# Kernel optimization log

Measured on AMD Instinct MI355X. Metric: run time of the kernel, lower is better.

Reference implementation:

```python
import jax, jax.numpy as jnp
import numpy as np

N, E, F_IN, HID, HEADS, NCLS, NG = 50000, 800000, 128, 128, 4, 10, 512
C = HID // HEADS          # per-head channels
BN_EPS = 1e-5
NEG_SLOPE = 0.2           # SuperGATConv default negative_slope
N_CONV = 3


def setup_inputs() -> dict:
    key = jax.random.key(0)
    ks = jax.random.split(key, 16)
    x = jax.random.normal(ks[0], (N, F_IN), jnp.float32)
    # edges with no self loops (reference appends self loops itself, as SuperGATConv does)
    src = jax.random.randint(ks[1], (E,), 0, N, dtype=jnp.int32)
    off = jax.random.randint(ks[2], (E,), 1, N, dtype=jnp.int32)
    dst = (src + off) % N
    edge_index = jnp.stack([src, dst], axis=0)
    batch = jnp.sort(jax.random.randint(ks[3], (N,), 0, NG, dtype=jnp.int32))
    s = 0.1
    # BatchNorm params per module init: weight=1, bias=1e-4 (running stats fresh: mean=0, var=1)
    inp = {
        "x": x, "edge_index": edge_index, "batch": batch,
        "bn_feat_g": jnp.ones((F_IN,), jnp.float32), "bn_feat_b": jnp.full((F_IN,), 1e-4, jnp.float32),
        "w_feat": jax.random.normal(ks[4], (F_IN, HID), jnp.float32) * s,
        "b_feat": jnp.zeros((HID,), jnp.float32),
        "bn_conv_g": jnp.ones((N_CONV, HID), jnp.float32), "bn_conv_b": jnp.full((N_CONV, HID), 1e-4, jnp.float32),
        "w_gat": jax.random.normal(ks[5], (N_CONV, HID, HID), jnp.float32) * s,
        "att_l": jax.random.normal(ks[6], (N_CONV, HEADS, C), jnp.float32) * s,
        "att_r": jax.random.normal(ks[7], (N_CONV, HEADS, C), jnp.float32) * s,
        "b_gat": jnp.zeros((N_CONV, HID), jnp.float32),
        "bn_fc_g": jnp.ones((HID,), jnp.float32), "bn_fc_b": jnp.full((HID,), 1e-4, jnp.float32),
        "w_fc": jax.random.normal(ks[8], (HID, HID), jnp.float32) * s,
        "b_fc": jnp.zeros((HID,), jnp.float32),
        "bn_hid_g": jnp.ones((HID,), jnp.float32), "bn_hid_b": jnp.full((HID,), 1e-4, jnp.float32),
        "w_cls": jax.random.normal(ks[9], (HID, NCLS), jnp.float32) * s,
        "b_cls": jnp.zeros((NCLS,), jnp.float32),
    }
    return inp


def _bn_eval(h, g, b):
    # eval-mode BatchNorm1d with fresh running stats (mean=0, var=1)
    return h * (g / jnp.sqrt(1.0 + BN_EPS)) + b


def _segment_softmax(a, seg, num_segments):
    # softmax over edges grouped by destination node (PyG softmax semantics)
    m = jax.ops.segment_max(a, seg, num_segments=num_segments)
    a = jnp.exp(a - m[seg])
    s = jax.ops.segment_sum(a, seg, num_segments=num_segments)
    return a / (s[seg] + 1e-16)


def _supergat_mx(h, src, dst, W, att_l, att_r, bias):
    # h: [N, HID] -> per-head features [N, H, C]
    hh = (h @ W).reshape(N, HEADS, C)
    h_j = hh[src]  # source (message) features  [E2, H, C]
    h_i = hh[dst]  # destination features       [E2, H, C]
    logits = jnp.einsum('ehc,ehc->eh', h_i, h_j)                       # MX dot-product
    alpha = jnp.einsum('ehc,hc->eh', h_j, att_l) + jnp.einsum('ehc,hc->eh', h_i, att_r)
    alpha = alpha * jax.nn.sigmoid(logits)
    alpha = jax.nn.leaky_relu(alpha, NEG_SLOPE)
    alpha = _segment_softmax(alpha, dst, N)                            # [E2, H]
    out = jax.ops.segment_sum(h_j * alpha[..., None], dst, num_segments=N)
    return out.reshape(N, HID) + bias


def reference(x, edge_index, batch, bn_feat_g, bn_feat_b, w_feat, b_feat,
              bn_conv_g, bn_conv_b, w_gat, att_l, att_r, b_gat,
              bn_fc_g, bn_fc_b, w_fc, b_fc, bn_hid_g, bn_hid_b, w_cls, b_cls):
    loops = jnp.arange(N, dtype=edge_index.dtype)
    src = jnp.concatenate([edge_index[0], loops])   # SuperGATConv adds self loops
    dst = jnp.concatenate([edge_index[1], loops])
    h = _bn_eval(x, bn_feat_g, bn_feat_b)
    h = jax.nn.relu(h @ w_feat + b_feat)            # GCNConv(gfn=True) == Linear
    for i in range(N_CONV):
        h = _bn_eval(h, bn_conv_g[i], bn_conv_b[i])
        h = jax.nn.relu(_supergat_mx(h, src, dst, w_gat[i], att_l[i], att_r[i], b_gat[i]))
    g = jax.ops.segment_sum(h, batch, num_segments=NG)  # global_add_pool -> [NG, HID]
    g = _bn_eval(g, bn_fc_g, bn_fc_b)
    g = jax.nn.relu(g @ w_fc + b_fc)
    g = _bn_eval(g, bn_hid_g, bn_hid_b)
    logits = g @ w_cls + b_cls
    att_loss = jnp.float32(0.0)  # eval mode: no edge-sampled attention loss
    return jax.nn.log_softmax(logits, axis=-1), att_loss
```

## Files before the change

### kernel.cpp

```cpp
#include <hip/hip_runtime.h>

#define NN 50000
#define EE 800000
#define FHID 128
#define NHEAD 4
#define NGRAPH 512
#define NCLS 10
#define BK 256
#define BCH 4096
#define NBLK_E 196
#define NBUCK 196
#define CAPB 6144

typedef unsigned short u16;
typedef unsigned int u32;
typedef unsigned long long u64;
typedef __attribute__((ext_vector_type(8))) short bf16x8;
typedef __attribute__((ext_vector_type(4))) float f32x4;

__device__ __forceinline__ float bf2f(u16 u){
    union { u32 i; float f; } v; v.i = ((u32)u) << 16; return v.f;
}
__device__ __forceinline__ float bflo(u32 u){
    union { u32 i; float f; } v; v.i = u << 16; return v.f;
}
__device__ __forceinline__ float bfhi(u32 u){
    union { u32 i; float f; } v; v.i = u & 0xffff0000u; return v.f;
}
__device__ __forceinline__ u16 f2bf(float f){
    union { float f; u32 i; } v; v.f = f;
    u32 r = v.i + 0x7fffu + ((v.i >> 16) & 1u);
    return (u16)(r >> 16);
}
__device__ __forceinline__ u32 pack2(float a, float b){
    return ((u32)f2bf(b) << 16) | f2bf(a);
}
__device__ __forceinline__ float loadF(const void* p, int i, int isf32){
    return isf32 ? ((const float*)p)[i] : bf2f(((const u16*)p)[i]);
}
__device__ __forceinline__ void unpk8(uint4 v, float* f){
    f[0]=bflo(v.x); f[1]=bfhi(v.x);
    f[2]=bflo(v.y); f[3]=bfhi(v.y);
    f[4]=bflo(v.z); f[5]=bfhi(v.z);
    f[6]=bflo(v.w); f[7]=bfhi(v.w);
}

__device__ int detect_local(const u16* x, int tid, int nthreads, int* lds){
    int ok = 0;
    for (int i = tid; i < 1024; i += nthreads){
        u16 u = x[i];
        int e = (u >> 7) & 0xFF;
        if ((u & 0x7fff) == 0 || (e >= 0x70 && e <= 0x85)) ok++;
    }
    lds[tid] = ok;
    __syncthreads();
    for (int o2 = nthreads >> 1; o2 > 0; o2 >>= 1){
        if (tid < o2) lds[tid] += lds[tid + o2];
        __syncthreads();
    }
    int r = (lds[0] < 900) ? 1 : 0;
    __syncthreads();
    return r;
}

__global__ __launch_bounds__(256) void prep_all(
        const u16* __restrict__ xz,
        const void* w_feat, const void* b_feat, const void* bn_feat_g, const void* bn_feat_b,
        const void* w_gat, const void* bn_conv_g, const void* bn_conv_b, const void* b_gat,
        const void* wfc, const void* bfc, const void* bnfg, const void* bnfb,
        const void* bnhg, const void* bnhb, const void* wcls, const void* bcls,
        const void* attl, const void* attr,
        u16* __restrict__ Wt, float* __restrict__ cvec, float* __restrict__ biasv,
        float* __restrict__ hp, int* __restrict__ dflag, int* __restrict__ gcur)
{
    __shared__ int ldsi[256];
    __shared__ float red[128];
    int bid = blockIdx.x, t = threadIdx.x;
    int isf32 = detect_local(xz, t, 256, ldsi);
    if (bid == 0){
        if (t == 0) dflag[0] = isf32;
        gcur[t] = t * CAPB;
    }

    if (bid < 512){
        if (t >= 128) return;
        int L = bid >> 7;
        int n = bid & 127;
        int k = t;
        const float rs = rsqrtf(1.0f + 1e-5f);
        float wv, bg, bb;
        if (L == 0){
            wv = loadF(w_feat, k*FHID + n, isf32);
            bg = loadF(bn_feat_g, k, isf32);
            bb = loadF(bn_feat_b, k, isf32);
        } else {
            wv = loadF(w_gat, (L-1)*FHID*FHID + k*FHID + n, isf32);
            bg = loadF(bn_conv_g, (L-1)*FHID + k, isf32);
            bb = loadF(bn_conv_b, (L-1)*FHID + k, isf32);
        }
        Wt[L*FHID*FHID + n*FHID + k] = f2bf(bg * rs * wv);
        red[k] = bb * wv;
        __syncthreads();
        for (int o2 = 64; o2 > 0; o2 >>= 1){
            if (k < o2) red[k] += red[k + o2];
            __syncthreads();
        }
        if (k == 0){
            float c = red[0];
            if (L == 0) c += loadF(b_feat, n, isf32);
            cvec[L*FHID + n] = c;
            if (L > 0) biasv[L*FHID + n] = loadF(b_gat, (L-1)*FHID + n, isf32);
        }
    } else {
        int gt = (bid - 512)*256 + t;
        for (int i = gt; i < FHID*FHID; i += 16*256) hp[i] = loadF(wfc, i, isf32);
        if (gt < FHID*NCLS) hp[16384 + gt] = loadF(wcls, gt, isf32);
        if (gt >= 2048 && gt < 2048 + 3*FHID){
            int i = gt - 2048;
            hp[18320 + i] = loadF(attl, i, isf32);
            hp[18704 + i] = loadF(attr, i, isf32);
        }
        if (gt >= 2560 && gt < 2560 + FHID){
            int tt = gt - 2560;
            hp[17664 + tt] = loadF(bnfg, tt, isf32);
            hp[17792 + tt] = loadF(bnfb, tt, isf32);
            hp[17920 + tt] = loadF(bfc,  tt, isf32);
            hp[18048 + tt] = loadF(bnhg, tt, isf32);
            hp[18176 + tt] = loadF(bnhb, tt, isf32);
        }
        if (gt >= 3072 && gt < 3072 + NCLS) hp[18304 + (gt - 3072)] = loadF(bcls, gt - 3072, isf32);
    }
}

__global__ __launch_bounds__(256) void gemm128(const void* __restrict__ A,
                                               const u16* __restrict__ Wt,
                                               const float* __restrict__ cvec,
                                               u16* __restrict__ out, int relu,
                                               int araw, const int* __restrict__ flag,
                                               const float* __restrict__ attl,
                                               const float* __restrict__ attr,
                                               float* __restrict__ al,
                                               float* __restrict__ ar)
{
    int wave = threadIdx.x >> 6;
    int lane = threadIdx.x & 63;
    int m = lane & 15, quad = lane >> 4;
    int rowbase = blockIdx.x * 128 + wave * 32;
    bool f32in = araw && flag[0];
    const u16*  Au = (const u16*)A;
    const float* Af = (const float*)A;
    int r0 = rowbase + m, r1 = rowbase + 16 + m;
    bool v0 = r0 < NN, v1 = r1 < NN;
    f32x4 acc[2][8];
#pragma unroll
    for (int i = 0; i < 2; i++)
#pragma unroll
        for (int j = 0; j < 8; j++) acc[i][j] = (f32x4){0.f,0.f,0.f,0.f};
#pragma unroll
    for (int t = 0; t < 4; t++){
        bf16x8 a0 = {0,0,0,0,0,0,0,0}, a1 = {0,0,0,0,0,0,0,0};
        int kof = t*32 + quad*8;
        if (f32in){
            if (v0){
                const float* p = Af + (size_t)r0*FHID + kof;
                float4 u0 = *(const float4*)p, u1 = *(const float4*)(p+4);
                a0[0]=(short)f2bf(u0.x); a0[1]=(short)f2bf(u0.y);
                a0[2]=(short)f2bf(u0.z); a0[3]=(short)f2bf(u0.w);
                a0[4]=(short)f2bf(u1.x); a0[5]=(short)f2bf(u1.y);
                a0[6]=(short)f2bf(u1.z); a0[7]=(short)f2bf(u1.w);
            }
            if (v1){
                const float* p = Af + (size_t)r1*FHID + kof;
                float4 u0 = *(const float4*)p, u1 = *(const float4*)(p+4);
                a1[0]=(short)f2bf(u0.x); a1[1]=(short)f2bf(u0.y);
                a1[2]=(short)f2bf(u0.z); a1[3]=(short)f2bf(u0.w);
                a1[4]=(short)f2bf(u1.x); a1[5]=(short)f2bf(u1.y);
                a1[6]=(short)f2bf(u1.z); a1[7]=(short)f2bf(u1.w);
            }
        } else {
            if (v0) a0 = *(const bf16x8*)(Au + (size_t)r0*FHID + kof);
            if (v1) a1 = *(const bf16x8*)(Au + (size_t)r1*FHID + kof);
        }
#pragma unroll
        for (int ct = 0; ct < 8; ct++){
            bf16x8 wfrag = *(const bf16x8*)(Wt + (ct*16 + m)*FHID + kof);
            acc[0][ct] = __builtin_amdgcn_mfma_f32_16x16x32_bf16(wfrag, a0, acc[0][ct], 0, 0, 0);
            acc[1][ct] = __builtin_amdgcn_mfma_f32_16x16x32_bf16(wfrag, a1, acc[1][ct], 0, 0, 0);
        }
    }
    bool doa = (attl != nullptr);
#pragma unroll
    for (int tt = 0; tt < 2; tt++){
        int row = rowbase + tt*16 + m;
        bool rv = row < NN;
        float sl[4] = {0.f,0.f,0.f,0.f};
        float sr[4] = {0.f,0.f,0.f,0.f};
#pragma unroll
        for (int ct = 0; ct < 8; ct++){
            int cb = ct*16 + quad*4;
            float4 cv = *(const float4*)(cvec + cb);
            float w0 = acc[tt][ct][0] + cv.x;
            float w1 = acc[tt][ct][1] + cv.y;
            float w2 = acc[tt][ct][2] + cv.z;
            float w3 = acc[tt][ct][3] + cv.w;
            if (relu){
                w0 = fmaxf(w0, 0.f); w1 = fmaxf(w1, 0.f);
                w2 = fmaxf(w2, 0.f); w3 = fmaxf(w3, 0.f);
            }
            if (doa){
                int h = ct >> 1;
                float4 tl = *(const float4*)(attl + cb);
                float4 tr = *(const float4*)(attr + cb);
                sl[h] += w0*tl.x + w1*tl.y + w2*tl.z + w3*tl.w;
                sr[h] += w0*tr.x + w1*tr.y + w2*tr.z + w3*tr.w;
            }
            if (rv){
                uint2 st; st.x = pack2(w0, w1); st.y = pack2(w2, w3);
                *(uint2*)(out + (size_t)row*FHID + cb) = st;
            }
        }
        if (doa){
#pragma unroll
            for (int h = 0; h < 4; h++){
                sl[h] += __shfl_xor(sl[h], 16, 64);
                sl[h] += __shfl_xor(sl[h], 32, 64);
                sr[h] += __shfl_xor(sr[h], 16, 64);
                sr[h] += __shfl_xor(sr[h], 32, 64);
            }
            if (rv){
                al[row*NHEAD + quad] = sl[quad];
                ar[row*NHEAD + quad] = sr[quad];
            }
        }
    }
}

__global__ __launch_bounds__(256) void bin_edges(const int* __restrict__ srcp,
        const int* __restrict__ dstp, int* __restrict__ gcur, u64* __restrict__ binned)
{
    __shared__ int h[BK], lb[BK], gb[BK], cur[BK];
    __shared__ u64 stage[BCH];
    int t = threadIdx.x;
    h[t] = 0;
    __syncthreads();
    int base = blockIdx.x * BCH;
    int sv[16], dv[16];
#pragma unroll
    for (int k = 0; k < 16; k++){
        int e = base + k*256 + t;
        int d = -1, s = 0;
        if (e < EE){
            d = dstp[e]; s = srcp[e];
            if ((u32)d >= NN) d = -1;
        }
        sv[k] = s; dv[k] = d;
        if (d >= 0) atomicAdd(&h[d >> 8], 1);
    }
    __syncthreads();
    lb[t] = h[t];
    __syncthreads();
    for (int off = 1; off < BK; off <<= 1){
        int x = (t >= off) ? lb[t - off] : 0;
        __syncthreads();
        lb[t] += x;
        __syncthreads();
    }
    int excl = lb[t] - h[t];
    int tot  = lb[BK-1];
    __syncthreads();
    lb[t] = excl;
    gb[t] = h[t] ? atomicAdd(&gcur[t], h[t]) : 0;
    cur[t] = 0;
    __syncthreads();
#pragma unroll
    for (int k = 0; k < 16; k++){
        int d = dv[k];
        if (d >= 0){
            int b = d >> 8;
            int p = lb[b] + atomicAdd(&cur[b], 1);
            stage[p] = ((u64)(u32)d << 32) | (u32)sv[k];
        }
    }
    __syncthreads();
    for (int i = t; i < tot; i += 256){
        u64 pr = stage[i];
        int b = (int)(pr >> 40);
        binned[gb[b] + (i - lb[b])] = pr;
    }
}

__global__ __launch_bounds__(256) void build_csr(const u64* __restrict__ binned,
        const int* __restrict__ gcur, int2* __restrict__ rowdeg, int* __restrict__ colbuf)
{
    __shared__ int deg[BK], ls[BK], cur[BK];
    __shared__ int colstage[CAPB];
    int b = blockIdx.x, t = threadIdx.x;
    int gb = b * CAPB;
    int cnt = gcur[b] - gb;
    if (cnt < 0) cnt = 0;
    if (cnt > CAPB) cnt = CAPB;
    deg[t] = 0;
    __syncthreads();
    for (int i = t; i < cnt; i += 256){
        int d = (int)(binned[gb + i] >> 32);
        atomicAdd(&deg[d & 255], 1);
    }
    __syncthreads();
    ls[t] = deg[t];
    __syncthreads();
    for (int off = 1; off < BK; off <<= 1){
        int x = (t >= off) ? ls[t - off] : 0;
        __syncthreads();
        ls[t] += x;
        __syncthreads();
    }
    int excl = ls[t] - deg[t];
    int node = b*256 + t;
    if (node < NN) rowdeg[node] = (int2){gb + excl, gb + excl + deg[t]};
    cur[t] = excl;
    __syncthreads();
    for (int i = t; i < cnt; i += 256){
        u64 pr = binned[gb + i];
        int d = (int)(pr >> 32) & 255;
        int s = (int)(u32)pr;
        int p = atomicAdd(&cur[d], 1);
        colstage[p] = s;
    }
    __syncthreads();
    for (int i = t; i < cnt; i += 256) colbuf[gb + i] = colstage[i];
}

__global__ __launch_bounds__(256) void supergat_conv(const u16* __restrict__ hh,
        const float* __restrict__ al, const float* __restrict__ ar,
        const int2* __restrict__ rowdeg, const int* __restrict__ colbuf,
        const float* __restrict__ bias, u16* __restrict__ hout)
{
    int wid  = (blockIdx.x*256 + threadIdx.x) >> 6;
    int lane = threadIdx.x & 63;
    int group = lane >> 4;
    int gl    = lane & 15;
    int head  = gl >> 2;
    int q     = gl & 3;
    int node  = wid*4 + group;
    bool valid = node < NN;
    int snode = valid ? node : 0;
    int chbase = head*32 + q*8;

    uint4 hdv = *(const uint4*)(hh + (size_t)snode*FHID + chbase);
    float hd[8]; unpk8(hdv, hd);
    float arn = ar[snode*NHEAD + head];
    float aln = al[snode*NHEAD + head];

    float d = hd[0]*hd[0]+hd[1]*hd[1]+hd[2]*hd[2]+hd[3]*hd[3]
            + hd[4]*hd[4]+hd[5]*hd[5]+hd[6]*hd[6]+hd[7]*hd[7];
    d += __shfl_xor(d, 1, 64);
    d += __shfl_xor(d, 2, 64);
    float a = (aln + arn) * (1.0f / (1.0f + __expf(-d)));
    a = (a > 0.0f) ? a : 0.2f*a;
    float p = __expf(fminf(a, 60.f));
    float s = p;
    float o[8];
#pragma unroll
    for (int i = 0; i < 8; i++) o[i] = p*hd[i];

    int2 rd = valid ? rowdeg[node] : (int2){0,0};
    int e0 = rd.x, e1 = rd.y;
    if (e0 < 0) e0 = 0;
    if (e1 > BK*CAPB) e1 = BK*CAPB;

    int e = e0;
    while (e + 3 < e1){
        int sidx[4]; uint4 xv[4]; float af[4];
#pragma unroll
        for (int j = 0; j < 4; j++){
            int si = colbuf[e + j];
            if ((u32)si >= NN) si = 0;
            sidx[j] = si;
        }
#pragma unroll
        for (int j = 0; j < 4; j++){
            xv[j] = *(const uint4*)(hh + (size_t)sidx[j]*FHID + chbase);
            af[j] = al[sidx[j]*NHEAD + head];
        }
#pragma unroll
        for (int j = 0; j < 4; j++){
            float hs[8]; unpk8(xv[j], hs);
            float lg = hd[0]*hs[0]+hd[1]*hs[1]+hd[2]*hs[2]+hd[3]*hs[3]
                     + hd[4]*hs[4]+hd[5]*hs[5]+hd[6]*hs[6]+hd[7]*hs[7];
            lg += __shfl_xor(lg, 1, 64);
            lg += __shfl_xor(lg, 2, 64);
            float a2 = (af[j] + arn) * (1.0f / (1.0f + __expf(-lg)));
            a2 = (a2 > 0.0f) ? a2 : 0.2f*a2;
            float pe = __expf(fminf(a2, 60.f));
            s += pe;
#pragma unroll
            for (int i = 0; i < 8; i++) o[i] += pe*hs[i];
        }
        e += 4;
    }
    while (e < e1){
        int si = colbuf[e];
        if ((u32)si >= NN) si = 0;
        uint4 x1 = *(const uint4*)(hh + (size_t)si*FHID + chbase);
        float af1 = al[si*NHEAD + head];
        float hs[8]; unpk8(x1, hs);
        float lg = hd[0]*hs[0]+hd[1]*hs[1]+hd[2]*hs[2]+hd[3]*hs[3]
                 + hd[4]*hs[4]+hd[5]*hs[5]+hd[6]*hs[6]+hd[7]*hs[7];
        lg += __shfl_xor(lg, 1, 64);
        lg += __shfl_xor(lg, 2, 64);
        float a2 = (af1 + arn) * (1.0f / (1.0f + __expf(-lg)));
        a2 = (a2 > 0.0f) ? a2 : 0.2f*a2;
        float pe = __expf(fminf(a2, 60.f));
        s += pe;
#pragma unroll
        for (int i = 0; i < 8; i++) o[i] += pe*hs[i];
        e++;
    }

    if (valid){
        float inv = 1.0f / (s + 1e-16f);
        uint4 w;
        w.x = pack2(fmaxf(o[0]*inv + bias[chbase+0], 0.f),
                    fmaxf(o[1]*inv + bias[chbase+1], 0.f));
        w.y = pack2(fmaxf(o[2]*inv + bias[chbase+2], 0.f),
                    fmaxf(o[3]*inv + bias[chbase+3], 0.f));
        w.z = pack2(fmaxf(o[4]*inv + bias[chbase+4], 0.f),
                    fmaxf(o[5]*inv + bias[chbase+5], 0.f));
        w.w = pack2(fmaxf(o[6]*inv + bias[chbase+6], 0.f),
                    fmaxf(o[7]*inv + bias[chbase+7], 0.f));
        *(uint4*)(hout + (size_t)node*FHID + chbase) = w;
    }
}

__global__ void pool_head(const u16* __restrict__ h, const int* __restrict__ batch,
                          const float* __restrict__ hp, const int* __restrict__ flag,
                          void* __restrict__ out)
{
    __shared__ int bounds[2];
    __shared__ float gb[FHID];
    __shared__ float g2[FHID];
    __shared__ float lg[16];
    int gi = blockIdx.x, t = threadIdx.x;
    int isf32 = flag[0];
    if (t < 2){
        int target = gi + t;
        int lo = 0, hi = NN;
        while (lo < hi){
            int mid = (lo + hi) >> 1;
            if (batch[mid] < target) lo = mid + 1; else hi = mid;
        }
        bounds[t] = lo;
    }
    __syncthreads();
    float acc0 = 0.f;
    for (int node = bounds[0]; node < bounds[1]; node++)
        acc0 += bf2f(h[(size_t)node*FHID + t]);
    const float rs = rsqrtf(1.0f + 1e-5f);
    gb[t] = acc0 * (hp[17664 + t] * rs) + hp[17792 + t];
    __syncthreads();
    float acc = hp[17920 + t];
    for (int k = 0; k < FHID; k++) acc += gb[k] * hp[k*FHID + t];
    acc = fmaxf(acc, 0.f);
    g2[t] = acc * (hp[18048 + t] * rs) + hp[18176 + t];
    __syncthreads();
    if (t < NCLS){
        float l = hp[18304 + t];
        for (int k = 0; k < FHID; k++) l += g2[k] * hp[16384 + k*NCLS + t];
        lg[t] = l;
    }
    __syncthreads();
    if (t == 0){
        float mx = lg[0];
        for (int j = 1; j < NCLS; j++) mx = fmaxf(mx, lg[j]);
        float se = 0.f;
        for (int j = 0; j < NCLS; j++) se += __expf(lg[j] - mx);
        float lse = logf(se) + mx;
        if (isf32){
            float* o = (float*)out;
            for (int j = 0; j < NCLS; j++) o[gi*NCLS + j] = lg[j] - lse;
            if (gi == 0) o[NGRAPH*NCLS] = 0.f;
        } else {
            u16* o = (u16*)out;
            for (int j = 0; j < NCLS; j++) o[gi*NCLS + j] = f2bf(lg[j] - lse);
            if (gi == 0) o[NGRAPH*NCLS] = 0;
        }
    }
}

extern "C" void kernel_launch(void* const* d_in, const int* in_sizes, int n_in,
                              void* d_out, int out_size, void* d_ws, size_t ws_size,
                              hipStream_t stream)
{
    (void)in_sizes; (void)n_in; (void)out_size; (void)ws_size;
    const void* x         = d_in[0];
    const int* edge       = (const int*)d_in[1];
    const int* batch      = (const int*)d_in[2];

    char* ws = (char*)d_ws;
    size_t off = 0;
    auto alloc = [&](size_t bytes) -> char* {
        char* p = ws + off; off += (bytes + 255) & ~(size_t)255; return p;
    };
    int*   dflag   = (int*)  alloc(256);
    u16*   WtAll   = (u16*)  alloc((size_t)4*FHID*FHID*2);
    float* cvecAll = (float*)alloc((size_t)4*FHID*4);
    float* biasv   = (float*)alloc((size_t)4*FHID*4);
    float* headp   = (float*)alloc((size_t)19088*4);
    float* al      = (float*)alloc((size_t)NN*NHEAD*4);
    float* ar      = (float*)alloc((size_t)NN*NHEAD*4);
    int*   gcur    = (int*)  alloc((size_t)BK*4);
    int2*  rowdeg  = (int2*) alloc((size_t)NN*8);
    int*   colbuf  = (int*)  alloc((size_t)BK*CAPB*4);
    u16*   hA      = (u16*)  alloc((size_t)NN*FHID*2);
    u16*   hB      = (u16*)  alloc((size_t)NN*FHID*2);
    u64*   binned  = (u64*)hB;

    const int* srcp = edge;
    const int* dstp = edge + EE;

    prep_all<<<528, 256, 0, stream>>>((const u16*)x,
        d_in[5], d_in[6], d_in[3], d_in[4], d_in[9], d_in[7], d_in[8], d_in[12],
        d_in[15], d_in[16], d_in[13], d_in[14], d_in[17], d_in[18], d_in[19], d_in[20],
        d_in[10], d_in[11],
        WtAll, cvecAll, biasv, headp, dflag, gcur);

    bin_edges<<<NBLK_E, 256, 0, stream>>>(srcp, dstp, gcur, binned);
    build_csr<<<NBUCK, 256, 0, stream>>>(binned, gcur, rowdeg, colbuf);

    gemm128<<<(NN + 127)/128, 256, 0, stream>>>(x, WtAll, cvecAll, hA, 1, 1, dflag,
                                                nullptr, nullptr, nullptr, nullptr);

    for (int i = 0; i < 3; i++){
        gemm128<<<(NN + 127)/128, 256, 0, stream>>>(hA, WtAll + (i+1)*FHID*FHID,
                                                    cvecAll + (i+1)*FHID, hB, 0, 0, dflag,
                                                    headp + 18320 + i*FHID,
                                                    headp + 18704 + i*FHID, al, ar);
        supergat_conv<<<(NN + 15)/16, 256, 0, stream>>>(hB, al, ar, rowdeg, colbuf,
                                                        biasv + (i+1)*FHID, hA);
    }

    pool_head<<<NGRAPH, 128, 0, stream>>>(hA, batch, headp, dflag, d_out);
}
```

Baseline: 388.3 us.

## Fuse edge binning into prep kernel, pack edges to 32 bits, shrink GEMM tiles

Edge binning now runs as extra blocks of the parameter-prep kernel, which removes one launch. Each block writes its bucket histogram to a partition table instead of reserving space through global atomics. build_csr prefix-sums those per-block counts and gathers its bucket's edges with a binary search. Each edge is packed into a u32 holding the 16-bit source and 8-bit local destination, which halves binned traffic but relies on N fitting in 16 bits. The GEMM now processes 64 rows per block instead of 128, giving more blocks and fewer accumulators per thread at the cost of more weight-fragment reloads.

```diff
diff --git a/kernel.cpp b/kernel.cpp
--- a/kernel.cpp
+++ b/kernel.cpp
@@ -14,7 +14,6 @@
 
 typedef unsigned short u16;
 typedef unsigned int u32;
-typedef unsigned long long u64;
 typedef __attribute__((ext_vector_type(8))) short bf16x8;
 typedef __attribute__((ext_vector_type(4))) float f32x4;
 
@@ -45,16 +44,16 @@
     f[6]=bflo(v.w); f[7]=bfhi(v.w);
 }
 
-__device__ int detect_local(const u16* x, int tid, int nthreads, int* lds){
+__device__ int detect_local(const u16* x, int tid, int* lds){
     int ok = 0;
-    for (int i = tid; i < 1024; i += nthreads){
+    for (int i = tid; i < 1024; i += 256){
         u16 u = x[i];
         int e = (u >> 7) & 0xFF;
         if ((u & 0x7fff) == 0 || (e >= 0x70 && e <= 0x85)) ok++;
     }
     lds[tid] = ok;
     __syncthreads();
-    for (int o2 = nthreads >> 1; o2 > 0; o2 >>= 1){
+    for (int o2 = 128; o2 > 0; o2 >>= 1){
         if (tid < o2) lds[tid] += lds[tid + o2];
         __syncthreads();
     }
@@ -63,73 +62,186 @@
     return r;
 }
 
-__global__ __launch_bounds__(256) void prep_all(
+__global__ __launch_bounds__(256) void prep_bin(
         const u16* __restrict__ xz,
         const void* w_feat, const void* b_feat, const void* bn_feat_g, const void* bn_feat_b,
         const void* w_gat, const void* bn_conv_g, const void* bn_conv_b, const void* b_gat,
         const void* wfc, const void* bfc, const void* bnfg, const void* bnfb,
         const void* bnhg, const void* bnhb, const void* wcls, const void* bcls,
         const void* attl, const void* attr,
+        const int* __restrict__ srcp, const int* __restrict__ dstp,
         u16* __restrict__ Wt, float* __restrict__ cvec, float* __restrict__ biasv,
-        float* __restrict__ hp, int* __restrict__ dflag, int* __restrict__ gcur)
+        float* __restrict__ hp, int* __restrict__ dflag,
+        u32* __restrict__ binned, int* __restrict__ gpart)
 {
     __shared__ int ldsi[256];
     __shared__ float red[128];
+    __shared__ int h[BK], lb[BK], cur[BK];
+    __shared__ u32 stage[BCH];
     int bid = blockIdx.x, t = threadIdx.x;
-    int isf32 = detect_local(xz, t, 256, ldsi);
-    if (bid == 0){
-        if (t == 0) dflag[0] = isf32;
-        gcur[t] = t * CAPB;
-    }
-
-    if (bid < 512){
-        if (t >= 128) return;
-        int L = bid >> 7;
-        int n = bid & 127;
-        int k = t;
-        const float rs = rsqrtf(1.0f + 1e-5f);
-        float wv, bg, bb;
-        if (L == 0){
-            wv = loadF(w_feat, k*FHID + n, isf32);
-            bg = loadF(bn_feat_g, k, isf32);
-            bb = loadF(bn_feat_b, k, isf32);
+
+    if (bid < 528){
+        int isf32 = detect_local(xz, t, ldsi);
+        if (bid == 0 && t == 0) dflag[0] = isf32;
+        if (bid < 512){
+            if (t >= 128) return;
+            int L = bid >> 7;
+            int n = bid & 127;
+            int k = t;
+            const float rs = rsqrtf(1.0f + 1e-5f);
+            float wv, bg, bb;
+            if (L == 0){
+                wv = loadF(w_feat, k*FHID + n, isf32);
+                bg = loadF(bn_feat_g, k, isf32);
+                bb = loadF(bn_feat_b, k, isf32);
+            } else {
+                wv = loadF(w_gat, (L-1)*FHID*FHID + k*FHID + n, isf32);
+                bg = loadF(bn_conv_g, (L-1)*FHID + k, isf32);
+                bb = loadF(bn_conv_b, (L-1)*FHID + k, isf32);
+            }
+            Wt[L*FHID*FHID + n*FHID + k] = f2bf(bg * rs * wv);
+            red[k] = bb * wv;
+            __syncthreads();
+            for (int o2 = 64; o2 > 0; o2 >>= 1){
+                if (k < o2) red[k] += red[k + o2];
+                __syncthreads();
+            }
+            if (k == 0){
+                float c = red[0];
+                if (L == 0) c += loadF(b_feat, n, isf32);
+                cvec[L*FHID + n] = c;
+                if (L > 0) biasv[L*FHID + n] = loadF(b_gat, (L-1)*FHID + n, isf32);
+            }
         } else {
-            wv = loadF(w_gat, (L-1)*FHID*FHID + k*FHID + n, isf32);
-            bg = loadF(bn_conv_g, (L-1)*FHID + k, isf32);
-            bb = loadF(bn_conv_b, (L-1)*FHID + k, isf32);
-        }
-        Wt[L*FHID*FHID + n*FHID + k] = f2bf(bg * rs * wv);
-        red[k] = bb * wv;
+            int gt = (bid - 512)*256 + t;
+            for (int i = gt; i < FHID*FHID; i += 16*256) hp[i] = loadF(wfc, i, isf32);
+            if (gt < FHID*NCLS) hp[16384 + gt] = loadF(wcls, gt, isf32);
+            if (gt >= 2048 && gt < 2048 + 3*FHID){
+                int i = gt - 2048;
+                hp[18320 + i] = loadF(attl, i, isf32);
+                hp[18704 + i] = loadF(attr, i, isf32);
+            }
+            if (gt >= 2560 && gt < 2560 + FHID){
+                int tt = gt - 2560;
+                hp[17664 + tt] = loadF(bnfg, tt, isf32);
+                hp[17792 + tt] = loadF(bnfb, tt, isf32);
+                hp[17920 + tt] = loadF(bfc,  tt, isf32);
+                hp[18048 + tt] = loadF(bnhg, tt, isf32);
+                hp[18176 + tt] = loadF(bnhb, tt, isf32);
+            }
+            if (gt >= 3072 && gt < 3072 + NCLS)
+                hp[18304 + (gt - 3072)] = loadF(bcls, gt - 3072, isf32);
+        }
+        return;
+    }
+
+    int j = bid - 528;
+    h[t] = 0;
+    __syncthreads();
+    int base = j * BCH;
+    int sv[16], dv[16];
+#pragma unroll
+    for (int k = 0; k < 16; k++){
+        int e = base + k*256 + t;
+        int d = -1, s = 0;
+        if (e < EE){
+            d = dstp[e]; s = srcp[e];
+            if ((u32)d >= NN) d = -1;
+        }
+        sv[k] = s; dv[k] = d;
+        if (d >= 0) atomicAdd(&h[d >> 8], 1);
+    }
+    __syncthreads();
+    lb[t] = h[t];
+    __syncthreads();
+    for (int off = 1; off < BK; off <<= 1){
+        int x = (t >= off) ? lb[t - off] : 0;
         __syncthreads();
-        for (int o2 = 64; o2 > 0; o2 >>= 1){
-            if (k < o2) red[k] += red[k + o2];
-            __syncthreads();
-        }
-        if (k == 0){
-            float c = red[0];
-            if (L == 0) c += loadF(b_feat, n, isf32);
-            cvec[L*FHID + n] = c;
-            if (L > 0) biasv[L*FHID + n] = loadF(b_gat, (L-1)*FHID + n, isf32);
-        }
-    } else {
-        int gt = (bid - 512)*256 + t;
-        for (int i = gt; i < FHID*FHID; i += 16*256) hp[i] = loadF(wfc, i, isf32);
-        if (gt < FHID*NCLS) hp[16384 + gt] = loadF(wcls, gt, isf32);
-        if (gt >= 2048 && gt < 2048 + 3*FHID){
-            int i = gt - 2048;
-            hp[18320 + i] = loadF(attl, i, isf32);
-            hp[18704 + i] = loadF(attr, i, isf32);
-        }
-        if (gt >= 2560 && gt < 2560 + FHID){
-            int tt = gt - 2560;
-            hp[17664 + tt] = loadF(bnfg, tt, isf32);
-            hp[17792 + tt] = loadF(bnfb, tt, isf32);
-            hp[17920 + tt] = loadF(bfc,  tt, isf32);
-            hp[18048 + tt] = loadF(bnhg, tt, isf32);
-            hp[18176 + tt] = loadF(bnhb, tt, isf32);
-        }
-        if (gt >= 3072 && gt < 3072 + NCLS) hp[18304 + (gt - 3072)] = loadF(bcls, gt - 3072, isf32);
-    }
+        lb[t] += x;
+        __syncthreads();
+    }
+    int excl = lb[t] - h[t];
+    int tot  = lb[BK-1];
+    __syncthreads();
+    lb[t] = excl;
+    cur[t] = 0;
+    __syncthreads();
+#pragma unroll
+    for (int k = 0; k < 16; k++){
+        int d = dv[k];
+        if (d >= 0){
+            int b = d >> 8;
+            int p = lb[b] + atomicAdd(&cur[b], 1);
+            stage[p] = ((u32)(d & 255) << 16) | (u32)(sv[k] & 0xffff);
+        }
+    }
+    __syncthreads();
+    for (int i = t; i < tot; i += 256) binned[base + i] = stage[i];
+    gpart[j*BK + t] = h[t];
+}
+
+__global__ __launch_bounds__(256) void build_csr(const u32* __restrict__ binned,
+        const int* __restrict__ gpart, int2* __restrict__ rowdeg, int* __restrict__ colbuf)
+{
+    __shared__ int joff[NBLK_E], jdst[NBLK_E + 1];
+    __shared__ int deg[BK], ls[BK], cur[BK];
+    __shared__ u32 pstage[CAPB];
+    __shared__ u32 colstage[CAPB];
+    int b = blockIdx.x, t = threadIdx.x;
+    int gb = b * CAPB;
+
+    if (t < NBLK_E){
+        const int* gp = gpart + t*BK;
+        int offv = 0;
+        for (int u = 0; u < b; u++) offv += gp[u];
+        joff[t] = offv;
+        ls[t] = gp[b];
+    }
+    __syncthreads();
+    if (t == 0){
+        int run = 0;
+        for (int jj = 0; jj < NBLK_E; jj++){ jdst[jj] = run; run += ls[jj]; }
+        jdst[NBLK_E] = run;
+    }
+    __syncthreads();
+    int cnt = jdst[NBLK_E];
+    if (cnt > CAPB) cnt = CAPB;
+
+    for (int i = t; i < cnt; i += 256){
+        int lo = 0, hi = NBLK_E - 1;
+        while (lo < hi){
+            int mid = (lo + hi + 1) >> 1;
+            if (jdst[mid] <= i) lo = mid; else hi = mid - 1;
+        }
+        pstage[i] = binned[lo*BCH + joff[lo] + (i - jdst[lo])];
+    }
+    __syncthreads();
+    deg[t] = 0;
+    __syncthreads();
+    for (int i = t; i < cnt; i += 256)
+        atomicAdd(&deg[(pstage[i] >> 16) & 255], 1);
+    __syncthreads();
+    ls[t] = deg[t];
+    __syncthreads();
+    for (int off = 1; off < BK; off <<= 1){
+        int x = (t >= off) ? ls[t - off] : 0;
+        __syncthreads();
+        ls[t] += x;
+        __syncthreads();
+    }
+    int excl = ls[t] - deg[t];
+    int node = b*256 + t;
+    if (node < NN) rowdeg[node] = (int2){gb + excl, gb + excl + deg[t]};
+    cur[t] = excl;
+    __syncthreads();
+    for (int i = t; i < cnt; i += 256){
+        u32 pr = pstage[i];
+        int d = (pr >> 16) & 255;
+        int p = atomicAdd(&cur[d], 1);
+        colstage[p] = pr & 0xffffu;
+    }
+    __syncthreads();
+    for (int i = t; i < cnt; i += 256) colbuf[gb + i] = (int)colstage[i];
 }
 
 __global__ __launch_bounds__(256) void gemm128(const void* __restrict__ A,
@@ -145,189 +257,79 @@
     int wave = threadIdx.x >> 6;
     int lane = threadIdx.x & 63;
     int m = lane & 15, quad = lane >> 4;
-    int rowbase = blockIdx.x * 128 + wave * 32;
+    int rowbase = blockIdx.x * 64 + wave * 16;
     bool f32in = araw && flag[0];
     const u16*  Au = (const u16*)A;
     const float* Af = (const float*)A;
-    int r0 = rowbase + m, r1 = rowbase + 16 + m;
-    bool v0 = r0 < NN, v1 = r1 < NN;
-    f32x4 acc[2][8];
-#pragma unroll
-    for (int i = 0; i < 2; i++)
-#pragma unroll
-        for (int j = 0; j < 8; j++) acc[i][j] = (f32x4){0.f,0.f,0.f,0.f};
+    int arow = rowbase + m;
+    bool av = arow < NN;
+    f32x4 acc[8];
+#pragma unroll
+    for (int j = 0; j < 8; j++) acc[j] = (f32x4){0.f,0.f,0.f,0.f};
 #pragma unroll
     for (int t = 0; t < 4; t++){
-        bf16x8 a0 = {0,0,0,0,0,0,0,0}, a1 = {0,0,0,0,0,0,0,0};
+        bf16x8 a0 = {0,0,0,0,0,0,0,0};
         int kof = t*32 + quad*8;
         if (f32in){
-            if (v0){
-                const float* p = Af + (size_t)r0*FHID + kof;
+            if (av){
+                const float* p = Af + (size_t)arow*FHID + kof;
                 float4 u0 = *(const float4*)p, u1 = *(const float4*)(p+4);
                 a0[0]=(short)f2bf(u0.x); a0[1]=(short)f2bf(u0.y);
                 a0[2]=(short)f2bf(u0.z); a0[3]=(short)f2bf(u0.w);
                 a0[4]=(short)f2bf(u1.x); a0[5]=(short)f2bf(u1.y);
                 a0[6]=(short)f2bf(u1.z); a0[7]=(short)f2bf(u1.w);
             }
-            if (v1){
-                const float* p = Af + (size_t)r1*FHID + kof;
-                float4 u0 = *(const float4*)p, u1 = *(const float4*)(p+4);
-                a1[0]=(short)f2bf(u0.x); a1[1]=(short)f2bf(u0.y);
-                a1[2]=(short)f2bf(u0.z); a1[3]=(short)f2bf(u0.w);
-                a1[4]=(short)f2bf(u1.x); a1[5]=(short)f2bf(u1.y);
-                a1[6]=(short)f2bf(u1.z); a1[7]=(short)f2bf(u1.w);
-            }
         } else {
-            if (v0) a0 = *(const bf16x8*)(Au + (size_t)r0*FHID + kof);
-            if (v1) a1 = *(const bf16x8*)(Au + (size_t)r1*FHID + kof);
+            if (av) a0 = *(const bf16x8*)(Au + (size_t)arow*FHID + kof);
         }
 #pragma unroll
         for (int ct = 0; ct < 8; ct++){
             bf16x8 wfrag = *(const bf16x8*)(Wt + (ct*16 + m)*FHID + kof);
-            acc[0][ct] = __builtin_amdgcn_mfma_f32_16x16x32_bf16(wfrag, a0, acc[0][ct], 0, 0, 0);
-            acc[1][ct] = __builtin_amdgcn_mfma_f32_16x16x32_bf16(wfrag, a1, acc[1][ct], 0, 0, 0);
+            acc[ct] = __builtin_amdgcn_mfma_f32_16x16x32_bf16(wfrag, a0, acc[ct], 0, 0, 0);
         }
     }
     bool doa = (attl != nullptr);
-#pragma unroll
-    for (int tt = 0; tt < 2; tt++){
-        int row = rowbase + tt*16 + m;
-        bool rv = row < NN;
-        float sl[4] = {0.f,0.f,0.f,0.f};
-        float sr[4] = {0.f,0.f,0.f,0.f};
-#pragma unroll
-        for (int ct = 0; ct < 8; ct++){
-            int cb = ct*16 + quad*4;
-            float4 cv = *(const float4*)(cvec + cb);
-            float w0 = acc[tt][ct][0] + cv.x;
-            float w1 = acc[tt][ct][1] + cv.y;
-            float w2 = acc[tt][ct][2] + cv.z;
-            float w3 = acc[tt][ct][3] + cv.w;
-            if (relu){
-                w0 = fmaxf(w0, 0.f); w1 = fmaxf(w1, 0.f);
-                w2 = fmaxf(w2, 0.f); w3 = fmaxf(w3, 0.f);
-            }
-            if (doa){
-                int h = ct >> 1;
-                float4 tl = *(const float4*)(attl + cb);
-                float4 tr = *(const float4*)(attr + cb);
-                sl[h] += w0*tl.x + w1*tl.y + w2*tl.z + w3*tl.w;
-                sr[h] += w0*tr.x + w1*tr.y + w2*tr.z + w3*tr.w;
-            }
-            if (rv){
-                uint2 st; st.x = pack2(w0, w1); st.y = pack2(w2, w3);
-                *(uint2*)(out + (size_t)row*FHID + cb) = st;
-            }
+    int row = rowbase + m;
+    bool rv = row < NN;
+    float sl[4] = {0.f,0.f,0.f,0.f};
+    float sr[4] = {0.f,0.f,0.f,0.f};
+#pragma unroll
+    for (int ct = 0; ct < 8; ct++){
+        int cb = ct*16 + quad*4;
+        float4 cv = *(const float4*)(cvec + cb);
+        float w0 = acc[ct][0] + cv.x;
+        float w1 = acc[ct][1] + cv.y;
+        float w2 = acc[ct][2] + cv.z;
+        float w3 = acc[ct][3] + cv.w;
+        if (relu){
+            w0 = fmaxf(w0, 0.f); w1 = fmaxf(w1, 0.f);
+            w2 = fmaxf(w2, 0.f); w3 = fmaxf(w3, 0.f);
         }
         if (doa){
-#pragma unroll
-            for (int h = 0; h < 4; h++){
-                sl[h] += __shfl_xor(sl[h], 16, 64);
-                sl[h] += __shfl_xor(sl[h], 32, 64);
-                sr[h] += __shfl_xor(sr[h], 16, 64);
-                sr[h] += __shfl_xor(sr[h], 32, 64);
-            }
-            if (rv){
-                al[row*NHEAD + quad] = sl[quad];
-                ar[row*NHEAD + quad] = sr[quad];
-            }
-        }
-    }
-}
-
-__global__ __launch_bounds__(256) void bin_edges(const int* __restrict__ srcp,
-        const int* __restrict__ dstp, int* __restrict__ gcur, u64* __restrict__ binned)
-{
-    __shared__ int h[BK], lb[BK], gb[BK], cur[BK];
-    __shared__ u64 stage[BCH];
-    int t = threadIdx.x;
-    h[t] = 0;
-    __syncthreads();
-    int base = blockIdx.x * BCH;
-    int sv[16], dv[16];
-#pragma unroll
-    for (int k = 0; k < 16; k++){
-        int e = base + k*256 + t;
-        int d = -1, s = 0;
-        if (e < EE){
-            d = dstp[e]; s = srcp[e];
-            if ((u32)d >= NN) d = -1;
-        }
-        sv[k] = s; dv[k] = d;
-        if (d >= 0) atomicAdd(&h[d >> 8], 1);
-    }
-    __syncthreads();
-    lb[t] = h[t];
-    __syncthreads();
-    for (int off = 1; off < BK; off <<= 1){
-        int x = (t >= off) ? lb[t - off] : 0;
-        __syncthreads();
-        lb[t] += x;
-        __syncthreads();
-    }
-    int excl = lb[t] - h[t];
-    int tot  = lb[BK-1];
-    __syncthreads();
-    lb[t] = excl;
-    gb[t] = h[t] ? atomicAdd(&gcur[t], h[t]) : 0;
-    cur[t] = 0;
-    __syncthreads();
-#pragma unroll
-    for (int k = 0; k < 16; k++){
-        int d = dv[k];
-        if (d >= 0){
-            int b = d >> 8;
-            int p = lb[b] + atomicAdd(&cur[b], 1);
-            stage[p] = ((u64)(u32)d << 32) | (u32)sv[k];
-        }
-    }
-    __syncthreads();
-    for (int i = t; i < tot; i += 256){
-        u64 pr = stage[i];
-        int b = (int)(pr >> 40);
-        binned[gb[b] + (i - lb[b])] = pr;
-    }
-}
-
-__global__ __launch_bounds__(256) void build_csr(const u64* __restrict__ binned,
-        const int* __restrict__ gcur, int2* __restrict__ rowdeg, int* __restrict__ colbuf)
-{
-    __shared__ int deg[BK], ls[BK], cur[BK];
-    __shared__ int colstage[CAPB];
-    int b = blockIdx.x, t = threadIdx.x;
-    int gb = b * CAPB;
-    int cnt = gcur[b] - gb;
-    if (cnt < 0) cnt = 0;
-    if (cnt > CAPB) cnt = CAPB;
-    deg[t] = 0;
-    __syncthreads();
-    for (int i = t; i < cnt; i += 256){
-        int d = (int)(binned[gb + i] >> 32);
-        atomicAdd(&deg[d & 255], 1);
-    }
-    __syncthreads();
-    ls[t] = deg[t];
-    __syncthreads();
-    for (int off = 1; off < BK; off <<= 1){
-        int x = (t >= off) ? ls[t - off] : 0;
-        __syncthreads();
-        ls[t] += x;
-        __syncthreads();
-    }
-    int excl = ls[t] - deg[t];
-    int node = b*256 + t;
-    if (node < NN) rowdeg[node] = (int2){gb + excl, gb + excl + deg[t]};
-    cur[t] = excl;
-    __syncthreads();
-    for (int i = t; i < cnt; i += 256){
-        u64 pr = binned[gb + i];
-        int d = (int)(pr >> 32) & 255;
-        int s = (int)(u32)pr;
-        int p = atomicAdd(&cur[d], 1);
-        colstage[p] = s;
-    }
-    __syncthreads();
-    for (int i = t; i < cnt; i += 256) colbuf[gb + i] = colstage[i];
+            int h = ct >> 1;
+            float4 tl = *(const float4*)(attl + cb);
+            float4 tr = *(const float4*)(attr + cb);
+            sl[h] += w0*tl.x + w1*tl.y + w2*tl.z + w3*tl.w;
+            sr[h] += w0*tr.x + w1*tr.y + w2*tr.z + w3*tr.w;
+        }
+        if (rv){
+            uint2 st; st.x = pack2(w0, w1); st.y = pack2(w2, w3);
+            *(uint2*)(out + (size_t)row*FHID + cb) = st;
+        }
+    }
+    if (doa){
+#pragma unroll
+        for (int h = 0; h < 4; h++){
+            sl[h] += __shfl_xor(sl[h], 16, 64);
+            sl[h] += __shfl_xor(sl[h], 32, 64);
+            sr[h] += __shfl_xor(sr[h], 16, 64);
+            sr[h] += __shfl_xor(sr[h], 32, 64);
+        }
+        if (rv){
+            al[row*NHEAD + quad] = sl[quad];
+            ar[row*NHEAD + quad] = sr[quad];
+        }
+    }
 }
 
 __global__ __launch_bounds__(256) void supergat_conv(const u16* __restrict__ hh,
@@ -508,33 +510,32 @@
     float* headp   = (float*)alloc((size_t)19088*4);
     float* al      = (float*)alloc((size_t)NN*NHEAD*4);
     float* ar      = (float*)alloc((size_t)NN*NHEAD*4);
-    int*   gcur    = (int*)  alloc((size_t)BK*4);
+    int*   gpart   = (int*)  alloc((size_t)NBLK_E*BK*4);
     int2*  rowdeg  = (int2*) alloc((size_t)NN*8);
     int*   colbuf  = (int*)  alloc((size_t)BK*CAPB*4);
     u16*   hA      = (u16*)  alloc((size_t)NN*FHID*2);
     u16*   hB      = (u16*)  alloc((size_t)NN*FHID*2);
-    u64*   binned  = (u64*)hB;
+    u32*   binned  = (u32*)hB;
 
     const int* srcp = edge;
     const int* dstp = edge + EE;
 
-    prep_all<<<528, 256, 0, stream>>>((const u16*)x,
+    prep_bin<<<528 + NBLK_E, 256, 0, stream>>>((const u16*)x,
         d_in[5], d_in[6], d_in[3], d_in[4], d_in[9], d_in[7], d_in[8], d_in[12],
         d_in[15], d_in[16], d_in[13], d_in[14], d_in[17], d_in[18], d_in[19], d_in[20],
-        d_in[10], d_in[11],
-        WtAll, cvecAll, biasv, headp, dflag, gcur);
-
-    bin_edges<<<NBLK_E, 256, 0, stream>>>(srcp, dstp, gcur, binned);
-    build_csr<<<NBUCK, 256, 0, stream>>>(binned, gcur, rowdeg, colbuf);
-
-    gemm128<<<(NN + 127)/128, 256, 0, stream>>>(x, WtAll, cvecAll, hA, 1, 1, dflag,
-                                                nullptr, nullptr, nullptr, nullptr);
+        d_in[10], d_in[11], srcp, dstp,
+        WtAll, cvecAll, biasv, headp, dflag, binned, gpart);
+
+    build_csr<<<NBUCK, 256, 0, stream>>>(binned, gpart, rowdeg, colbuf);
+
+    gemm128<<<(NN + 63)/64, 256, 0, stream>>>(x, WtAll, cvecAll, hA, 1, 1, dflag,
+                                              nullptr, nullptr, nullptr, nullptr);
 
     for (int i = 0; i < 3; i++){
-        gemm128<<<(NN + 127)/128, 256, 0, stream>>>(hA, WtAll + (i+1)*FHID*FHID,
-                                                    cvecAll + (i+1)*FHID, hB, 0, 0, dflag,
-                                                    headp + 18320 + i*FHID,
-                                                    headp + 18704 + i*FHID, al, ar);
+        gemm128<<<(NN + 63)/64, 256, 0, stream>>>(hA, WtAll + (i+1)*FHID*FHID,
+                                                  cvecAll + (i+1)*FHID, hB, 0, 0, dflag,
+                                                  headp + 18320 + i*FHID,
+                                                  headp + 18704 + i*FHID, al, ar);
         supergat_conv<<<(NN + 15)/16, 256, 0, stream>>>(hB, al, ar, rowdeg, colbuf,
                                                         biasv + (i+1)*FHID, hA);
     }
```

New measurement: 424.5 us. 9.3% more time.
